# Optimization experiments

Hardware: AMD Instinct MI355X
Metric: run time of the kernel (lower is better)

The kernel has to match this reference:

```python
import jax, jax.numpy as jnp
import numpy as np
import math

B, T, C = 8, 1024, 1024
E, K = 8, 2
H = 4 * C


def new_gelu(x):
    # tanh-approx GELU, identical to the torch reference
    c = math.sqrt(2.0 / math.pi)
    return 0.5 * x * (1.0 + jnp.tanh(c * (x + 0.044715 * x ** 3)))


def setup_inputs() -> dict:
    key = jax.random.key(0)
    ks = jax.random.split(key, 4)
    x = jax.random.normal(ks[0], (B, T, C), dtype=jnp.float32)
    # router: nn.Linear(C, E, bias=False), weight [E, C], init std=0.02
    router_w = 0.02 * jax.random.normal(ks[1], (E, C), dtype=jnp.float32)
    # stacked expert MLP weights (bias=False): c_fc [E, C, H], c_proj [E, H, C]
    w_fc = 0.02 * jax.random.normal(ks[2], (E, C, H), dtype=jnp.float32)
    w_proj = 0.02 * jax.random.normal(ks[3], (E, H, C), dtype=jnp.float32)
    return {"x": x, "router_w": router_w, "w_fc": w_fc, "w_proj": w_proj}


def reference(x, router_w, w_fc, w_proj):
    n_expert = w_fc.shape[0]
    seq_rep = x.mean(axis=1)                                  # [B, C]
    router_logits = seq_rep @ router_w.T                      # [B, E]
    probs_full = jax.nn.softmax(router_logits.astype(jnp.float32), axis=-1)
    probs = probs_full.astype(x.dtype)
    weights, sel = jax.lax.top_k(probs, K)                    # [B, K]
    weights = weights / weights.sum(axis=-1, keepdims=True)

    # gather selected expert weights and run grouped dense MLPs
    w1 = w_fc[sel]                                            # [B, K, C, H]
    w2 = w_proj[sel]                                          # [B, K, H, C]
    h = new_gelu(jnp.einsum('btc,bkch->bkth', x, w1))         # [B, K, T, H]
    out_k = jnp.einsum('bkth,bkhc->bktc', h, w2)              # [B, K, T, C]
    final_output = jnp.einsum('bk,bktc->btc', weights, out_k)

    # load balancing loss
    Bf = jnp.asarray(x.shape[0], jnp.float32)
    expert_importance = probs_full.sum(axis=0) / Bf           # [E]
    is_assigned = jnp.zeros_like(probs_full).at[jnp.arange(x.shape[0])[:, None], sel].set(1.0)
    expert_load = is_assigned.sum(axis=0) / Bf                # [E]
    load_balancing_loss = n_expert * jnp.sum(expert_importance * expert_load)
    return final_output, load_balancing_loss
```

## Files before the change

kernel.cpp:

```cpp
#include <hip/hip_runtime.h>

#define B_ 8
#define T_ 1024
#define C_ 1024
#define E_ 8
#define H_ 4096

typedef float v4f __attribute__((ext_vector_type(4)));
typedef short v8s __attribute__((ext_vector_type(8)));

__device__ __forceinline__ unsigned short f2bf(float f) {
  union { float f; unsigned int u; } x; x.f = f;
  unsigned int r = x.u + 0x7fffu + ((x.u >> 16) & 1u);
  return (unsigned short)(r >> 16);
}

__device__ __forceinline__ void async_load16(const unsigned short* g, unsigned short* l) {
  __builtin_amdgcn_global_load_lds(
      (const __attribute__((address_space(1))) void*)g,
      (__attribute__((address_space(3))) void*)l, 16, 0, 0);
}


__global__ void k_meanpart(const float* __restrict__ x, float* __restrict__ part,
                           unsigned short* __restrict__ xb) {
  int b = blockIdx.x >> 5, tc = blockIdx.x & 31;
  int c4 = threadIdx.x * 4;
  const size_t base = (size_t)b * T_ * C_ + (size_t)tc * 32 * C_ + c4;
  const float* xp = x + base;
  v4f s = {0.f, 0.f, 0.f, 0.f};
  for (int t = 0; t < 32; ++t) {
    v4f v = *(const v4f*)(xp + (size_t)t * C_);
    s += v;
    ushort4 o;
    o.x = f2bf(v.x); o.y = f2bf(v.y); o.z = f2bf(v.z); o.w = f2bf(v.w);
    *(ushort4*)(xb + base + (size_t)t * C_) = o;
  }
  *(v4f*)(part + (size_t)(tc * B_ + b) * C_ + c4) = s;
}

__global__ void k_router(const float* __restrict__ part, const float* __restrict__ rw,
                         int* __restrict__ sel, float* __restrict__ wv,
                         float* __restrict__ loss_out) {
  __shared__ float seq[B_ * C_];
  __shared__ float red[B_ * E_][4];
  __shared__ float pr[B_][E_];
  __shared__ int ss[B_][2];
  const int tid = threadIdx.x;
  for (int idx = tid; idx < B_ * C_; idx += 256) {
    float s = 0.f;
#pragma unroll
    for (int tc = 0; tc < 32; ++tc) s += part[(size_t)tc * B_ * C_ + idx];
    seq[idx] = s * (1.0f / T_);
  }
  __syncthreads();
  {
    int pair = tid >> 2, sub = tid & 3;
    int b = pair >> 3, e = pair & 7;
    float acc = 0.f;
    const float* sp = seq + b * C_ + sub * 256;
    const float* wp = rw + e * C_ + sub * 256;
    for (int c = 0; c < 256; ++c) acc += sp[c] * wp[c];
    red[pair][sub] = acc;
  }
  __syncthreads();
  if (tid < B_ * E_)
    pr[tid >> 3][tid & 7] = red[tid][0] + red[tid][1] + red[tid][2] + red[tid][3];
  __syncthreads();
  if (tid < B_) {
    int b = tid;
    float mx = pr[b][0];
#pragma unroll
    for (int e = 1; e < E_; ++e) mx = fmaxf(mx, pr[b][e]);
    float p[E_]; float sum = 0.f;
#pragma unroll
    for (int e = 0; e < E_; ++e) { p[e] = __expf(pr[b][e] - mx); sum += p[e]; }
    float inv = 1.0f / sum;
#pragma unroll
    for (int e = 0; e < E_; ++e) { p[e] *= inv; pr[b][e] = p[e]; }
    int i0 = 0;
#pragma unroll
    for (int e = 1; e < E_; ++e) if (p[e] > p[i0]) i0 = e;
    int i1 = (i0 == 0) ? 1 : 0;
#pragma unroll
    for (int e = 0; e < E_; ++e) if (e != i0 && p[e] > p[i1]) i1 = e;
    float s2 = p[i0] + p[i1];
    sel[b * 2 + 0] = i0; sel[b * 2 + 1] = i1;
    wv[b * 2 + 0] = p[i0] / s2; wv[b * 2 + 1] = p[i1] / s2;
    ss[b][0] = i0; ss[b][1] = i1;
  }
  __syncthreads();
  if (tid == 0) {
    float loss = 0.f;
    for (int e = 0; e < E_; ++e) {
      float imp = 0.f, ld = 0.f;
      for (int b = 0; b < B_; ++b) {
        imp += pr[b][e];
        ld += ((ss[b][0] == e) || (ss[b][1] == e)) ? 1.f : 0.f;
      }
      loss += (imp / (float)B_) * (ld / (float)B_);
    }
    loss_out[0] = loss * (float)E_;
  }
}

__global__ void k_transpose(const float* __restrict__ src, unsigned short* __restrict__ dst,
                            int R, int Cc) {
  __shared__ float tile[64][65];
  const size_t sl = (size_t)blockIdx.z * R * Cc;
  int c0 = blockIdx.x * 64, r0 = blockIdx.y * 64;
  int tx = threadIdx.x & 15, ty = threadIdx.x >> 4;
#pragma unroll
  for (int p = 0; p < 4; ++p) {
    int r = p * 16 + ty;
    v4f v = *(const v4f*)(src + sl + (size_t)(r0 + r) * Cc + c0 + tx * 4);
    tile[r][tx * 4 + 0] = v.x; tile[r][tx * 4 + 1] = v.y;
    tile[r][tx * 4 + 2] = v.z; tile[r][tx * 4 + 3] = v.w;
  }
  __syncthreads();
#pragma unroll
  for (int p = 0; p < 4; ++p) {
    int c = p * 16 + ty;
    int rr = tx * 4;
    ushort4 o;
    o.x = f2bf(tile[rr + 0][c]); o.y = f2bf(tile[rr + 1][c]);
    o.z = f2bf(tile[rr + 2][c]); o.w = f2bf(tile[rr + 3][c]);
    *(ushort4*)(dst + sl + (size_t)(c0 + c) * R + r0 + rr) = o;
  }
}


__device__ __forceinline__ void gemm_seg(const unsigned short* A, int lda,
                                         const unsigned short* Bt, int ldb,
                                         int Kd, int row0, int col0,
                                         unsigned short* As, unsigned short* Bs,
                                         v4f (&acc)[4][4]) {
  const int tid = threadIdx.x;
  const int lane = tid & 63;
  const int wave = __builtin_amdgcn_readfirstlane(tid >> 6);
  const int r = lane & 15, q = lane >> 4;
  const int wm = wave & 1, wn = wave >> 1;
  const int qs = q ^ ((r >> 1) & 3);
  const int lrow = lane >> 2;
  const int lch = (lane & 3) ^ ((lane >> 3) & 3);
  const bool doA = (wave < 2);
  const int jb = (wave & 1) * 4;
  const int gld = doA ? lda : ldb;
  const unsigned short* gbase =
      (doA ? (A + (size_t)row0 * lda) : (Bt + (size_t)col0 * ldb)) +
      (size_t)(jb * 16 + lrow) * gld + lch * 8;
  unsigned short* lbase = (doA ? As : Bs) + jb * 512;

  for (int kc = 0; kc < Kd; kc += 32) {
    const unsigned short* g = gbase + kc;
    async_load16(g + 0 * 16 * (size_t)gld, lbase + 0 * 512);
    async_load16(g + 1 * 16 * (size_t)gld, lbase + 1 * 512);
    async_load16(g + 2 * 16 * (size_t)gld, lbase + 2 * 512);
    async_load16(g + 3 * 16 * (size_t)gld, lbase + 3 * 512);
    __syncthreads();
    v8s af[4], bf[4];
#pragma unroll
    for (int i = 0; i < 4; ++i)
      af[i] = *(const v8s*)&As[((wm * 64 + i * 16 + r) * 4 + qs) * 8];
#pragma unroll
    for (int j = 0; j < 4; ++j)
      bf[j] = *(const v8s*)&Bs[((wn * 64 + j * 16 + r) * 4 + qs) * 8];
#pragma unroll
    for (int i = 0; i < 4; ++i)
#pragma unroll
      for (int j = 0; j < 4; ++j)
        acc[i][j] = __builtin_amdgcn_mfma_f32_16x16x32_bf16(af[i], bf[j], acc[i][j], 0, 0, 0);
    __syncthreads();
  }
}

__global__ __launch_bounds__(256, 4) void k_gemm1(
    const unsigned short* __restrict__ Xb, const unsigned short* __restrict__ Wfct,
    const int* __restrict__ sel, const float* __restrict__ wv,
    unsigned short* __restrict__ Hout) {
  __shared__ unsigned short SH[128 * 64];
  unsigned short* As = SH;
  unsigned short* Bs = SH + 128 * 32;
  const int bk = blockIdx.z;
  const int e = sel[bk];
  const float wgt = wv[bk];
  const int row0 = blockIdx.y * 128, col0 = blockIdx.x * 128;
  v4f acc[4][4];
#pragma unroll
  for (int i = 0; i < 4; ++i)
#pragma unroll
    for (int j = 0; j < 4; ++j) acc[i][j] = (v4f){0.f, 0.f, 0.f, 0.f};

  gemm_seg(Xb + (size_t)(bk >> 1) * T_ * C_, C_, Wfct + (size_t)e * H_ * C_, C_,
           C_, row0, col0, As, Bs, acc);

  const int tid = threadIdx.x;
  const int lane = tid & 63;
  const int wave = tid >> 6;
  const int r = lane & 15, q = lane >> 4;
  const int wm = wave & 1, wn = wave >> 1;
  unsigned short* Co = Hout + (size_t)bk * T_ * H_;
#pragma unroll
  for (int hh = 0; hh < 2; ++hh) {
    if (wm == hh) {
#pragma unroll
      for (int i = 0; i < 4; ++i)
#pragma unroll
        for (int j = 0; j < 4; ++j)
#pragma unroll
          for (int p = 0; p < 4; ++p) {
            int lr = i * 16 + q * 4 + p;
            int lc = wn * 64 + j * 16 + r;
            float u = acc[i][j][p];
            float y = 0.7978845608028654f * (u + 0.044715f * u * u * u);
            float t = 1.0f - 2.0f / (__expf(2.0f * y) + 1.0f);
            SH[lr * 128 + lc] = f2bf(0.5f * u * (1.0f + t) * wgt);
          }
    }
    __syncthreads();
#pragma unroll
    for (int it = 0; it < 4; ++it) {
      int idx = it * 256 + tid;
      int row = idx >> 4, ch = idx & 15;
      *(v8s*)&Co[(size_t)(row0 + hh * 64 + row) * H_ + col0 + ch * 8] =
          *(const v8s*)&SH[row * 128 + ch * 8];
    }
    __syncthreads();
  }
}

__global__ __launch_bounds__(256, 4) void k_gemm2(
    const unsigned short* __restrict__ Hin, const unsigned short* __restrict__ Wpt,
    const int* __restrict__ sel, float* __restrict__ P0, float* __restrict__ P1) {
  __shared__ unsigned short SH[128 * 64];
  unsigned short* As = SH;
  unsigned short* Bs = SH + 128 * 32;
  const int bk = blockIdx.z;
  const int b = bk >> 1, k = bk & 1;
  const int e = sel[bk];
  const int row0 = blockIdx.y * 128, col0 = blockIdx.x * 128;
  v4f acc[4][4];
#pragma unroll
  for (int i = 0; i < 4; ++i)
#pragma unroll
    for (int j = 0; j < 4; ++j) acc[i][j] = (v4f){0.f, 0.f, 0.f, 0.f};

  gemm_seg(Hin + (size_t)bk * T_ * H_, H_, Wpt + (size_t)e * C_ * H_, H_,
           H_, row0, col0, As, Bs, acc);

  const int lane = threadIdx.x & 63;
  const int wave = threadIdx.x >> 6;
  const int r = lane & 15, q = lane >> 4;
  const int wm = wave & 1, wn = wave >> 1;
  float* Co = (k == 0 ? P0 : P1) + (size_t)b * T_ * C_;
#pragma unroll
  for (int i = 0; i < 4; ++i) {
    int gr = row0 + wm * 64 + i * 16 + q * 4;
#pragma unroll
    for (int j = 0; j < 4; ++j) {
      int gc = col0 + wn * 64 + j * 16 + r;
#pragma unroll
      for (int p = 0; p < 4; ++p)
        Co[(size_t)(gr + p) * C_ + gc] = acc[i][j][p];
    }
  }
}

__global__ void k_add(float* __restrict__ out, const float* __restrict__ p1) {
  size_t i = ((size_t)blockIdx.x * 256 + threadIdx.x) * 4;
  v4f a = *(const v4f*)(out + i);
  v4f b = *(const v4f*)(p1 + i);
  a += b;
  *(v4f*)(out + i) = a;
}


extern "C" void kernel_launch(void* const* d_in, const int* in_sizes, int n_in,
                              void* d_out, int out_size, void* d_ws, size_t ws_size,
                              hipStream_t stream) {
  const float* x   = (const float*)d_in[0];
  const float* rw  = (const float*)d_in[1];
  const float* wfc = (const float*)d_in[2];
  const float* wpj = (const float*)d_in[3];
  float* out = (float*)d_out;
  char* ws = (char*)d_ws;

  float*          part = (float*)(ws + 0);
  int*            sel  = (int*)(ws + 1048576);
  float*          wv   = (float*)(ws + 1048576 + 64);
  unsigned short* xb   = (unsigned short*)(ws + 2097152);
  unsigned short* wfct = (unsigned short*)(ws + 2097152 + 16777216);
  unsigned short* wpjt = (unsigned short*)(ws + 2097152 + 16777216 + 67108864);
  unsigned short* h    = (unsigned short*)(ws + 2097152 + 16777216 + 2*67108864ll);
  float*          p1   = (float*)(ws + 2097152);

  k_meanpart<<<dim3(B_ * 32), dim3(256), 0, stream>>>(x, part, xb);
  k_router<<<dim3(1), dim3(256), 0, stream>>>(part, rw, sel, wv,
                                              out + (size_t)B_ * T_ * C_);
  k_transpose<<<dim3(H_ / 64, C_ / 64, E_), dim3(256), 0, stream>>>(wfc, wfct, C_, H_);
  k_transpose<<<dim3(C_ / 64, H_ / 64, E_), dim3(256), 0, stream>>>(wpj, wpjt, H_, C_);

  k_gemm1<<<dim3(H_ / 128, T_ / 128, B_ * 2), dim3(256), 0, stream>>>(xb, wfct, sel, wv, h);
  k_gemm2<<<dim3(C_ / 128, T_ / 128, B_ * 2), dim3(256), 0, stream>>>(h, wpjt, sel, out, p1);
  k_add<<<dim3(B_ * T_ * C_ / 4 / 256), dim3(256), 0, stream>>>(out, p1);
}
```

Measured before the change: 757.9 us.

## Replace 128x128 GEMM tiles with double-buffered 256x256 tiles and block swizzle

Both expert GEMMs move from 128x128 tiles (256 threads, single-buffered K=32 steps) to 256x256 tiles with 512 threads, K=128 chunks and a double-buffered 128KB LDS ring. Global-to-LDS async loads for the next chunk are interleaved with MFMA quadrants using explicit vmcnt and lgkmcnt waits, barriers and setprio, so memory latency overlaps compute. Block indices are XCD-swizzled to improve L2 reuse of expert weights. The larger tiles cut redundant global traffic per FLOP, at the cost of fewer blocks (occupancy) and more fragile hand scheduling.

Measured after the change: 653.4 us. 13.8% less time.

```diff
diff --git a/kernel.cpp b/kernel.cpp
--- a/kernel.cpp
+++ b/kernel.cpp
@@ -130,135 +130,191 @@
 }
 
 
-__device__ __forceinline__ void gemm_seg(const unsigned short* A, int lda,
-                                         const unsigned short* Bt, int ldb,
-                                         int Kd, int row0, int col0,
-                                         unsigned short* As, unsigned short* Bs,
-                                         v4f (&acc)[4][4]) {
+#define BARv() __builtin_amdgcn_s_barrier()
+#define LGK0() asm volatile("s_waitcnt lgkmcnt(0)" ::: "memory")
+#define VMC4() asm volatile("s_waitcnt vmcnt(4)" ::: "memory")
+#define VMC0() asm volatile("s_waitcnt vmcnt(0)" ::: "memory")
+
+__device__ __forceinline__ void gemm256(const unsigned short* __restrict__ Ag,
+                                        const unsigned short* __restrict__ Bg,
+                                        int lda, int ldb, int Kd,
+                                        unsigned short* LDS, v4f (&acc)[8][4]) {
   const int tid = threadIdx.x;
   const int lane = tid & 63;
-  const int wave = __builtin_amdgcn_readfirstlane(tid >> 6);
-  const int r = lane & 15, q = lane >> 4;
-  const int wm = wave & 1, wn = wave >> 1;
-  const int qs = q ^ ((r >> 1) & 3);
-  const int lrow = lane >> 2;
-  const int lch = (lane & 3) ^ ((lane >> 3) & 3);
-  const bool doA = (wave < 2);
-  const int jb = (wave & 1) * 4;
-  const int gld = doA ? lda : ldb;
-  const unsigned short* gbase =
-      (doA ? (A + (size_t)row0 * lda) : (Bt + (size_t)col0 * ldb)) +
-      (size_t)(jb * 16 + lrow) * gld + lch * 8;
-  unsigned short* lbase = (doA ? As : Bs) + jb * 512;
-
-  for (int kc = 0; kc < Kd; kc += 32) {
-    const unsigned short* g = gbase + kc;
-    async_load16(g + 0 * 16 * (size_t)gld, lbase + 0 * 512);
-    async_load16(g + 1 * 16 * (size_t)gld, lbase + 1 * 512);
-    async_load16(g + 2 * 16 * (size_t)gld, lbase + 2 * 512);
-    async_load16(g + 3 * 16 * (size_t)gld, lbase + 3 * 512);
-    __syncthreads();
-    v8s af[4], bf[4];
-#pragma unroll
-    for (int i = 0; i < 4; ++i)
-      af[i] = *(const v8s*)&As[((wm * 64 + i * 16 + r) * 4 + qs) * 8];
-#pragma unroll
-    for (int j = 0; j < 4; ++j)
-      bf[j] = *(const v8s*)&Bs[((wn * 64 + j * 16 + r) * 4 + qs) * 8];
-#pragma unroll
-    for (int i = 0; i < 4; ++i)
-#pragma unroll
-      for (int j = 0; j < 4; ++j)
-        acc[i][j] = __builtin_amdgcn_mfma_f32_16x16x32_bf16(af[i], bf[j], acc[i][j], 0, 0, 0);
-    __syncthreads();
-  }
-}
-
-__global__ __launch_bounds__(256, 4) void k_gemm1(
+  const int w = __builtin_amdgcn_readfirstlane(tid >> 6);
+  const int wm = w >> 2, wn = w & 3;
+  const int rr = lane & 15, q = lane >> 4, s7 = rr & 7;
+  const int ck0 = (q ^ s7) * 8;
+  const int ck1 = ((4 | q) ^ s7) * 8;
+  const int aoff = wm * 8192 + rr * 64;
+  const int boff = 16384 + (wn >> 1) * 8192 + (wn & 1) * 4096 + rr * 64;
+  const int w8 = w * 8;
+  const int l3 = lane >> 3;
+  const int srow = w8 + l3;
+  const int sel8 = ((lane & 7) ^ l3) * 8;
+  v8s af[4][2], bfr[4][2];
+
+#define STG(gb, ld, reg) do { \
+    const unsigned short* _g = (gb) + (size_t)srow * (ld) + sel8; \
+    async_load16(_g, LDS + (reg) + w8 * 64); \
+    async_load16(_g + (size_t)64 * (ld), LDS + (reg) + 4096 + w8 * 64); \
+  } while (0)
+
+#define RDA(i2, qi, bs) do { \
+    af[i2][0] = *(const v8s*)&LDS[(bs) + aoff + ((qi)*4+(i2))*1024 + ck0]; \
+    af[i2][1] = *(const v8s*)&LDS[(bs) + aoff + ((qi)*4+(i2))*1024 + ck1]; \
+  } while (0)
+
+#define RDB(j, bs) do { \
+    bfr[j][0] = *(const v8s*)&LDS[(bs) + boff + (j)*1024 + ck0]; \
+    bfr[j][1] = *(const v8s*)&LDS[(bs) + boff + (j)*1024 + ck1]; \
+  } while (0)
+
+#define QUAD(qi, qj) do { \
+    __builtin_amdgcn_s_setprio(1); \
+    _Pragma("unroll") for (int _i = 0; _i < 4; ++_i) \
+    _Pragma("unroll") for (int _j = 0; _j < 2; ++_j) { \
+      acc[(qi)*4+_i][(qj)*2+_j] = __builtin_amdgcn_mfma_f32_16x16x32_bf16( \
+          af[_i][0], bfr[(qj)*2+_j][0], acc[(qi)*4+_i][(qj)*2+_j], 0, 0, 0); \
+      acc[(qi)*4+_i][(qj)*2+_j] = __builtin_amdgcn_mfma_f32_16x16x32_bf16( \
+          af[_i][1], bfr[(qj)*2+_j][1], acc[(qi)*4+_i][(qj)*2+_j], 0, 0, 0); \
+    } \
+    __builtin_amdgcn_s_setprio(0); \
+  } while (0)
+
+  STG(Ag, lda, 0);
+  STG(Ag + (size_t)128 * lda, lda, 8192);
+  STG(Bg, ldb, 16384);
+  STG(Bg + (size_t)128 * ldb, ldb, 24576);
+  STG(Bg + 64, ldb, 32768 + 16384);
+  STG(Bg + (size_t)128 * ldb + 64, ldb, 32768 + 24576);
+  VMC4();
+  BARv();
+
+  const int NI = Kd >> 7;
+  for (int I = 0; I < NI; ++I) {
+    const int k0 = I << 7;
+    const bool last = (I == NI - 1);
+    RDA(0,0,0); RDA(1,0,0); RDA(2,0,0); RDA(3,0,0); RDB(0,0); RDB(1,0);
+    STG(Ag + k0 + 64, lda, 32768 + 0);
+    BARv(); LGK0(); QUAD(0,0); BARv();
+    RDB(2,0); RDB(3,0);
+    STG(Ag + (size_t)128 * lda + k0 + 64, lda, 32768 + 8192);
+    BARv(); LGK0(); QUAD(0,1); BARv();
+    RDA(0,1,0); RDA(1,1,0); RDA(2,1,0); RDA(3,1,0);
+    if (!last) STG(Bg + k0 + 128, ldb, 16384);
+    BARv(); LGK0(); QUAD(1,0); BARv();
+    if (!last) STG(Bg + (size_t)128 * ldb + k0 + 128, ldb, 24576);
+    BARv(); LGK0(); QUAD(1,1);
+    if (last) { VMC0(); } else { VMC4(); }
+    BARv();
+    RDA(0,0,32768); RDA(1,0,32768); RDA(2,0,32768); RDA(3,0,32768);
+    RDB(0,32768); RDB(1,32768);
+    if (!last) STG(Ag + k0 + 128, lda, 0);
+    BARv(); LGK0(); QUAD(0,0); BARv();
+    RDB(2,32768); RDB(3,32768);
+    if (!last) STG(Ag + (size_t)128 * lda + k0 + 128, lda, 8192);
+    BARv(); LGK0(); QUAD(0,1); BARv();
+    RDA(0,1,32768); RDA(1,1,32768); RDA(2,1,32768); RDA(3,1,32768);
+    if (!last) STG(Bg + k0 + 192, ldb, 32768 + 16384);
+    BARv(); LGK0(); QUAD(1,0); BARv();
+    if (!last) STG(Bg + (size_t)128 * ldb + k0 + 192, ldb, 32768 + 24576);
+    BARv(); LGK0(); QUAD(1,1);
+    if (!last) VMC4();
+    BARv();
+  }
+#undef STG
+#undef RDA
+#undef RDB
+#undef QUAD
+}
+
+__global__ __launch_bounds__(512, 2) void k_gemm1(
     const unsigned short* __restrict__ Xb, const unsigned short* __restrict__ Wfct,
     const int* __restrict__ sel, const float* __restrict__ wv,
     unsigned short* __restrict__ Hout) {
-  __shared__ unsigned short SH[128 * 64];
-  unsigned short* As = SH;
-  unsigned short* Bs = SH + 128 * 32;
-  const int bk = blockIdx.z;
+  __shared__ unsigned short LDS[65536];
+  int flat = blockIdx.x + 16 * (blockIdx.y + 4 * blockIdx.z);
+  int swz = (flat & 7) * 128 + (flat >> 3);
+  const int bx = swz & 15, by = (swz >> 4) & 3, bk = swz >> 6;
   const int e = sel[bk];
   const float wgt = wv[bk];
-  const int row0 = blockIdx.y * 128, col0 = blockIdx.x * 128;
-  v4f acc[4][4];
-#pragma unroll
-  for (int i = 0; i < 4; ++i)
+  const int row0 = by * 256, col0 = bx * 256;
+  v4f acc[8][4];
+#pragma unroll
+  for (int i = 0; i < 8; ++i)
 #pragma unroll
     for (int j = 0; j < 4; ++j) acc[i][j] = (v4f){0.f, 0.f, 0.f, 0.f};
 
-  gemm_seg(Xb + (size_t)(bk >> 1) * T_ * C_, C_, Wfct + (size_t)e * H_ * C_, C_,
-           C_, row0, col0, As, Bs, acc);
+  gemm256(Xb + (size_t)(bk >> 1) * T_ * C_ + (size_t)row0 * C_,
+          Wfct + (size_t)e * H_ * C_ + (size_t)col0 * C_,
+          C_, C_, C_, LDS, acc);
 
   const int tid = threadIdx.x;
   const int lane = tid & 63;
-  const int wave = tid >> 6;
-  const int r = lane & 15, q = lane >> 4;
-  const int wm = wave & 1, wn = wave >> 1;
+  const int w = tid >> 6, wm = w >> 2, wn = w & 3;
+  const int rr = lane & 15, q = lane >> 4;
   unsigned short* Co = Hout + (size_t)bk * T_ * H_;
 #pragma unroll
-  for (int hh = 0; hh < 2; ++hh) {
-    if (wm == hh) {
-#pragma unroll
-      for (int i = 0; i < 4; ++i)
+  for (int h = 0; h < 2; ++h) {
+    if (wm == h) {
+#pragma unroll
+      for (int i = 0; i < 8; ++i)
 #pragma unroll
         for (int j = 0; j < 4; ++j)
 #pragma unroll
           for (int p = 0; p < 4; ++p) {
             int lr = i * 16 + q * 4 + p;
-            int lc = wn * 64 + j * 16 + r;
+            int lc = wn * 64 + j * 16 + rr;
             float u = acc[i][j][p];
             float y = 0.7978845608028654f * (u + 0.044715f * u * u * u);
             float t = 1.0f - 2.0f / (__expf(2.0f * y) + 1.0f);
-            SH[lr * 128 + lc] = f2bf(0.5f * u * (1.0f + t) * wgt);
+            LDS[lr * 272 + lc] = f2bf(0.5f * u * (1.0f + t) * wgt);
           }
     }
     __syncthreads();
 #pragma unroll
-    for (int it = 0; it < 4; ++it) {
-      int idx = it * 256 + tid;
-      int row = idx >> 4, ch = idx & 15;
-      *(v8s*)&Co[(size_t)(row0 + hh * 64 + row) * H_ + col0 + ch * 8] =
-          *(const v8s*)&SH[row * 128 + ch * 8];
+    for (int m = 0; m < 8; ++m) {
+      int idx = m * 512 + tid;
+      int row = idx >> 5, cc = idx & 31;
+      *(v8s*)&Co[(size_t)(row0 + h * 128 + row) * H_ + col0 + cc * 8] =
+          *(const v8s*)&LDS[row * 272 + cc * 8];
     }
     __syncthreads();
   }
 }
 
-__global__ __launch_bounds__(256, 4) void k_gemm2(
+__global__ __launch_bounds__(512, 2) void k_gemm2(
     const unsigned short* __restrict__ Hin, const unsigned short* __restrict__ Wpt,
     const int* __restrict__ sel, float* __restrict__ P0, float* __restrict__ P1) {
-  __shared__ unsigned short SH[128 * 64];
-  unsigned short* As = SH;
-  unsigned short* Bs = SH + 128 * 32;
-  const int bk = blockIdx.z;
+  __shared__ unsigned short LDS[65536];
+  int flat = blockIdx.x + 4 * (blockIdx.y + 4 * blockIdx.z);
+  int swz = (flat & 7) * 32 + (flat >> 3);
+  const int bx = swz & 3, by = (swz >> 2) & 3, bk = swz >> 4;
   const int b = bk >> 1, k = bk & 1;
   const int e = sel[bk];
-  const int row0 = blockIdx.y * 128, col0 = blockIdx.x * 128;
-  v4f acc[4][4];
-#pragma unroll
-  for (int i = 0; i < 4; ++i)
+  const int row0 = by * 256, col0 = bx * 256;
+  v4f acc[8][4];
+#pragma unroll
+  for (int i = 0; i < 8; ++i)
 #pragma unroll
     for (int j = 0; j < 4; ++j) acc[i][j] = (v4f){0.f, 0.f, 0.f, 0.f};
 
-  gemm_seg(Hin + (size_t)bk * T_ * H_, H_, Wpt + (size_t)e * C_ * H_, H_,
-           H_, row0, col0, As, Bs, acc);
-
-  const int lane = threadIdx.x & 63;
-  const int wave = threadIdx.x >> 6;
-  const int r = lane & 15, q = lane >> 4;
-  const int wm = wave & 1, wn = wave >> 1;
+  gemm256(Hin + (size_t)bk * T_ * H_ + (size_t)row0 * H_,
+          Wpt + (size_t)e * C_ * H_ + (size_t)col0 * H_,
+          H_, H_, H_, LDS, acc);
+
+  const int tid = threadIdx.x;
+  const int lane = tid & 63;
+  const int w = tid >> 6, wm = w >> 2, wn = w & 3;
+  const int rr = lane & 15, q = lane >> 4;
   float* Co = (k == 0 ? P0 : P1) + (size_t)b * T_ * C_;
 #pragma unroll
-  for (int i = 0; i < 4; ++i) {
-    int gr = row0 + wm * 64 + i * 16 + q * 4;
+  for (int i = 0; i < 8; ++i) {
+    int gr = row0 + wm * 128 + i * 16 + q * 4;
 #pragma unroll
     for (int j = 0; j < 4; ++j) {
-      int gc = col0 + wn * 64 + j * 16 + r;
+      int gc = col0 + wn * 64 + j * 16 + rr;
 #pragma unroll
       for (int p = 0; p < 4; ++p)
         Co[(size_t)(gr + p) * C_ + gc] = acc[i][j][p];
@@ -300,7 +356,7 @@
   k_transpose<<<dim3(H_ / 64, C_ / 64, E_), dim3(256), 0, stream>>>(wfc, wfct, C_, H_);
   k_transpose<<<dim3(C_ / 64, H_ / 64, E_), dim3(256), 0, stream>>>(wpj, wpjt, H_, C_);
 
-  k_gemm1<<<dim3(H_ / 128, T_ / 128, B_ * 2), dim3(256), 0, stream>>>(xb, wfct, sel, wv, h);
-  k_gemm2<<<dim3(C_ / 128, T_ / 128, B_ * 2), dim3(256), 0, stream>>>(h, wpjt, sel, out, p1);
+  k_gemm1<<<dim3(H_ / 256, T_ / 256, B_ * 2), dim3(512), 0, stream>>>(xb, wfct, sel, wv, h);
+  k_gemm2<<<dim3(C_ / 256, T_ / 256, B_ * 2), dim3(512), 0, stream>>>(h, wpjt, sel, out, p1);
   k_add<<<dim3(B_ * T_ * C_ / 4 / 256), dim3(256), 0, stream>>>(out, p1);
 }
```

## Rewrite expert GEMMs with triple-buffered 128x256 tiles and fused expert-sum

Applied to the files above, without the earlier changes.

The GEMM core moves to a 512-thread, 128x256-tile kernel with K-step 64. It triple-buffers LDS with async global-to-LDS loads, explicit vmcnt waits and sched barriers, double-buffers fragments, and raises MFMA priority. Block indices are swizzled for L2 locality. gemm2 now accumulates both selected experts into one accumulator in a single block, which removes the partial buffer and the separate add kernel. The cost is a large LDS footprint (144KB) that limits occupancy, and each gemm2 block does twice the K work.

Result: faster. 716.7 us (-5.4%).

```diff
diff --git a/kernel.cpp b/kernel.cpp
--- a/kernel.cpp
+++ b/kernel.cpp
@@ -130,148 +130,171 @@
 }
 
 
-__device__ __forceinline__ void gemm_seg(const unsigned short* A, int lda,
-                                         const unsigned short* Bt, int ldb,
-                                         int Kd, int row0, int col0,
-                                         unsigned short* As, unsigned short* Bs,
-                                         v4f (&acc)[4][4]) {
+#define BAR()  __builtin_amdgcn_s_barrier()
+#define SCH0() __builtin_amdgcn_sched_barrier(0)
+
+__device__ __forceinline__ void gemm_core(const unsigned short* __restrict__ Ag,
+                                          const unsigned short* __restrict__ Bg,
+                                          int lda, int ldb, int Kd,
+                                          unsigned short* LDS, v4f (&acc)[4][4]) {
   const int tid = threadIdx.x;
   const int lane = tid & 63;
-  const int wave = __builtin_amdgcn_readfirstlane(tid >> 6);
-  const int r = lane & 15, q = lane >> 4;
-  const int wm = wave & 1, wn = wave >> 1;
-  const int qs = q ^ ((r >> 1) & 3);
-  const int lrow = lane >> 2;
-  const int lch = (lane & 3) ^ ((lane >> 3) & 3);
-  const bool doA = (wave < 2);
-  const int jb = (wave & 1) * 4;
-  const int gld = doA ? lda : ldb;
-  const unsigned short* gbase =
-      (doA ? (A + (size_t)row0 * lda) : (Bt + (size_t)col0 * ldb)) +
-      (size_t)(jb * 16 + lrow) * gld + lch * 8;
-  unsigned short* lbase = (doA ? As : Bs) + jb * 512;
-
-  for (int kc = 0; kc < Kd; kc += 32) {
-    const unsigned short* g = gbase + kc;
-    async_load16(g + 0 * 16 * (size_t)gld, lbase + 0 * 512);
-    async_load16(g + 1 * 16 * (size_t)gld, lbase + 1 * 512);
-    async_load16(g + 2 * 16 * (size_t)gld, lbase + 2 * 512);
-    async_load16(g + 3 * 16 * (size_t)gld, lbase + 3 * 512);
-    __syncthreads();
-    v8s af[4], bf[4];
-#pragma unroll
-    for (int i = 0; i < 4; ++i)
-      af[i] = *(const v8s*)&As[((wm * 64 + i * 16 + r) * 4 + qs) * 8];
-#pragma unroll
-    for (int j = 0; j < 4; ++j)
-      bf[j] = *(const v8s*)&Bs[((wn * 64 + j * 16 + r) * 4 + qs) * 8];
-#pragma unroll
-    for (int i = 0; i < 4; ++i)
-#pragma unroll
-      for (int j = 0; j < 4; ++j)
-        acc[i][j] = __builtin_amdgcn_mfma_f32_16x16x32_bf16(af[i], bf[j], acc[i][j], 0, 0, 0);
-    __syncthreads();
-  }
-}
-
-__global__ __launch_bounds__(256, 4) void k_gemm1(
+  const int w = __builtin_amdgcn_readfirstlane(tid >> 6);
+  const int wm = w >> 2, wn = w & 3;
+  const int rr = lane & 15, q = lane >> 4, s7 = rr & 7;
+  const int ck0 = (q ^ s7) * 8, ck1 = ((4 | q) ^ s7) * 8;
+  const int aof0 = wm * 4096 + rr * 64;
+  const int aof1 = aof0 + 1024, aof2 = aof0 + 2048, aof3 = aof0 + 3072;
+  const int bof0 = 8192 + wn * 4096 + rr * 64;
+  const int bof1 = bof0 + 1024, bof2 = bof0 + 2048, bof3 = bof0 + 3072;
+  const int srow = tid >> 3;
+  const int sc8 = ((tid & 7) ^ (srow & 7)) * 8;
+  const int ldst = tid * 8;
+  v8s a0[4], b0[4], a1[4], b1[4];
+
+#define STG1(goff, ld, loff) async_load16((goff) + (size_t)srow * (ld) + sc8, LDS + (loff) + ldst)
+#define STG6(kof, bb) do { \
+    STG1(Ag + (kof), lda, (bb)); \
+    STG1(Ag + (size_t)64 * lda + (kof), lda, (bb) + 4096); \
+    STG1(Bg + (kof), ldb, (bb) + 8192); \
+    STG1(Bg + (size_t)64 * ldb + (kof), ldb, (bb) + 12288); \
+    STG1(Bg + (size_t)128 * ldb + (kof), ldb, (bb) + 16384); \
+    STG1(Bg + (size_t)192 * ldb + (kof), ldb, (bb) + 20480); \
+  } while (0)
+#define RD8(A_, B_, bb, CK) do { \
+    A_[0] = *(const v8s*)&LDS[(bb) + aof0 + (CK)]; \
+    A_[1] = *(const v8s*)&LDS[(bb) + aof1 + (CK)]; \
+    A_[2] = *(const v8s*)&LDS[(bb) + aof2 + (CK)]; \
+    A_[3] = *(const v8s*)&LDS[(bb) + aof3 + (CK)]; \
+    B_[0] = *(const v8s*)&LDS[(bb) + bof0 + (CK)]; \
+    B_[1] = *(const v8s*)&LDS[(bb) + bof1 + (CK)]; \
+    B_[2] = *(const v8s*)&LDS[(bb) + bof2 + (CK)]; \
+    B_[3] = *(const v8s*)&LDS[(bb) + bof3 + (CK)]; \
+  } while (0)
+#define MM16(A_, B_) do { __builtin_amdgcn_s_setprio(1); \
+    _Pragma("unroll") for (int i_ = 0; i_ < 4; ++i_) \
+    _Pragma("unroll") for (int j_ = 0; j_ < 4; ++j_) \
+      acc[i_][j_] = __builtin_amdgcn_mfma_f32_16x16x32_bf16(A_[i_], B_[j_], acc[i_][j_], 0, 0, 0); \
+    __builtin_amdgcn_s_setprio(0); } while (0)
+
+  STG6(0, 0);
+  STG6(64, 24576);
+  asm volatile("s_waitcnt vmcnt(6)" ::: "memory");
+  BAR(); SCH0();
+  RD8(a0, b0, 0, ck0);
+
+  int bb0 = 0, bb1 = 24576, bb2 = 49152;
+  const int NT = Kd >> 6;
+#pragma unroll 1
+  for (int t = 0; t < NT; ++t) {
+    const bool n1 = (t + 1 < NT), s2 = (t + 2 < NT);
+    RD8(a1, b1, bb0, ck1);
+    SCH0();
+    if (n1) asm volatile("s_waitcnt vmcnt(0)" ::: "memory");
+    BAR(); SCH0();
+    if (s2) STG6((t + 2) * 64, bb2);
+    MM16(a0, b0);
+    SCH0();
+    if (n1) RD8(a0, b0, bb1, ck0);
+    SCH0();
+    MM16(a1, b1);
+    SCH0();
+    int tmp = bb0; bb0 = bb1; bb1 = bb2; bb2 = tmp;
+  }
+#undef STG1
+#undef STG6
+#undef RD8
+#undef MM16
+}
+
+__global__ __launch_bounds__(512, 2) void k_gemm1(
     const unsigned short* __restrict__ Xb, const unsigned short* __restrict__ Wfct,
     const int* __restrict__ sel, const float* __restrict__ wv,
     unsigned short* __restrict__ Hout) {
-  __shared__ unsigned short SH[128 * 64];
-  unsigned short* As = SH;
-  unsigned short* Bs = SH + 128 * 32;
-  const int bk = blockIdx.z;
+  __shared__ unsigned short LDS[73728];
+  int flat = blockIdx.x + 16 * (blockIdx.y + 8 * blockIdx.z);
+  int swz = (flat & 7) * 256 + (flat >> 3);
+  const int bx = swz & 15, by = (swz >> 4) & 7, bk = swz >> 7;
   const int e = sel[bk];
   const float wgt = wv[bk];
-  const int row0 = blockIdx.y * 128, col0 = blockIdx.x * 128;
+  const int row0 = by * 128, col0 = bx * 256;
   v4f acc[4][4];
 #pragma unroll
   for (int i = 0; i < 4; ++i)
 #pragma unroll
     for (int j = 0; j < 4; ++j) acc[i][j] = (v4f){0.f, 0.f, 0.f, 0.f};
 
-  gemm_seg(Xb + (size_t)(bk >> 1) * T_ * C_, C_, Wfct + (size_t)e * H_ * C_, C_,
-           C_, row0, col0, As, Bs, acc);
+  gemm_core(Xb + (size_t)(bk >> 1) * T_ * C_ + (size_t)row0 * C_,
+            Wfct + (size_t)e * H_ * C_ + (size_t)col0 * C_,
+            C_, C_, C_, LDS, acc);
 
   const int tid = threadIdx.x;
   const int lane = tid & 63;
-  const int wave = tid >> 6;
-  const int r = lane & 15, q = lane >> 4;
-  const int wm = wave & 1, wn = wave >> 1;
+  const int w = tid >> 6, wm = w >> 2, wn = w & 3;
+  const int rr = lane & 15, q = lane >> 4;
   unsigned short* Co = Hout + (size_t)bk * T_ * H_;
-#pragma unroll
-  for (int hh = 0; hh < 2; ++hh) {
-    if (wm == hh) {
-#pragma unroll
-      for (int i = 0; i < 4; ++i)
-#pragma unroll
-        for (int j = 0; j < 4; ++j)
-#pragma unroll
-          for (int p = 0; p < 4; ++p) {
-            int lr = i * 16 + q * 4 + p;
-            int lc = wn * 64 + j * 16 + r;
-            float u = acc[i][j][p];
-            float y = 0.7978845608028654f * (u + 0.044715f * u * u * u);
-            float t = 1.0f - 2.0f / (__expf(2.0f * y) + 1.0f);
-            SH[lr * 128 + lc] = f2bf(0.5f * u * (1.0f + t) * wgt);
-          }
-    }
-    __syncthreads();
-#pragma unroll
-    for (int it = 0; it < 4; ++it) {
-      int idx = it * 256 + tid;
-      int row = idx >> 4, ch = idx & 15;
-      *(v8s*)&Co[(size_t)(row0 + hh * 64 + row) * H_ + col0 + ch * 8] =
-          *(const v8s*)&SH[row * 128 + ch * 8];
-    }
-    __syncthreads();
-  }
-}
-
-__global__ __launch_bounds__(256, 4) void k_gemm2(
+  __syncthreads();
+#pragma unroll
+  for (int i = 0; i < 4; ++i)
+#pragma unroll
+    for (int j = 0; j < 4; ++j)
+#pragma unroll
+      for (int p = 0; p < 4; ++p) {
+        int lr = wm * 64 + i * 16 + q * 4 + p;
+        int lc = wn * 64 + j * 16 + rr;
+        float u = acc[i][j][p];
+        float y = 0.7978845608028654f * (u + 0.044715f * u * u * u);
+        float t = 1.0f - 2.0f / (__expf(2.0f * y) + 1.0f);
+        LDS[lr * 264 + lc] = f2bf(0.5f * u * (1.0f + t) * wgt);
+      }
+  __syncthreads();
+#pragma unroll
+  for (int m = 0; m < 8; ++m) {
+    int idx = m * 512 + tid;
+    int row = idx >> 5, ch = idx & 31;
+    *(v8s*)&Co[(size_t)(row0 + row) * H_ + col0 + ch * 8] =
+        *(const v8s*)&LDS[row * 264 + ch * 8];
+  }
+}
+
+__global__ __launch_bounds__(512, 2) void k_gemm2(
     const unsigned short* __restrict__ Hin, const unsigned short* __restrict__ Wpt,
-    const int* __restrict__ sel, float* __restrict__ P0, float* __restrict__ P1) {
-  __shared__ unsigned short SH[128 * 64];
-  unsigned short* As = SH;
-  unsigned short* Bs = SH + 128 * 32;
-  const int bk = blockIdx.z;
-  const int b = bk >> 1, k = bk & 1;
-  const int e = sel[bk];
-  const int row0 = blockIdx.y * 128, col0 = blockIdx.x * 128;
+    const int* __restrict__ sel, float* __restrict__ out) {
+  __shared__ unsigned short LDS[73728];
+  int flat = blockIdx.x + 4 * (blockIdx.y + 8 * blockIdx.z);
+  int swz = (flat & 7) * 32 + (flat >> 3);
+  const int bx = swz & 3, by = (swz >> 2) & 7, b = swz >> 5;
+  const int row0 = by * 128, col0 = bx * 256;
   v4f acc[4][4];
 #pragma unroll
   for (int i = 0; i < 4; ++i)
 #pragma unroll
     for (int j = 0; j < 4; ++j) acc[i][j] = (v4f){0.f, 0.f, 0.f, 0.f};
 
-  gemm_seg(Hin + (size_t)bk * T_ * H_, H_, Wpt + (size_t)e * C_ * H_, H_,
-           H_, row0, col0, As, Bs, acc);
-
-  const int lane = threadIdx.x & 63;
-  const int wave = threadIdx.x >> 6;
-  const int r = lane & 15, q = lane >> 4;
-  const int wm = wave & 1, wn = wave >> 1;
-  float* Co = (k == 0 ? P0 : P1) + (size_t)b * T_ * C_;
+  gemm_core(Hin + (size_t)(2 * b) * T_ * H_ + (size_t)row0 * H_,
+            Wpt + (size_t)sel[2 * b] * C_ * H_ + (size_t)col0 * H_,
+            H_, H_, H_, LDS, acc);
+  __syncthreads();
+  gemm_core(Hin + (size_t)(2 * b + 1) * T_ * H_ + (size_t)row0 * H_,
+            Wpt + (size_t)sel[2 * b + 1] * C_ * H_ + (size_t)col0 * H_,
+            H_, H_, H_, LDS, acc);
+
+  const int tid = threadIdx.x;
+  const int lane = tid & 63;
+  const int w = tid >> 6, wm = w >> 2, wn = w & 3;
+  const int rr = lane & 15, q = lane >> 4;
+  float* Co = out + (size_t)b * T_ * C_;
 #pragma unroll
   for (int i = 0; i < 4; ++i) {
     int gr = row0 + wm * 64 + i * 16 + q * 4;
 #pragma unroll
     for (int j = 0; j < 4; ++j) {
-      int gc = col0 + wn * 64 + j * 16 + r;
+      int gc = col0 + wn * 64 + j * 16 + rr;
 #pragma unroll
       for (int p = 0; p < 4; ++p)
         Co[(size_t)(gr + p) * C_ + gc] = acc[i][j][p];
     }
   }
-}
-
-__global__ void k_add(float* __restrict__ out, const float* __restrict__ p1) {
-  size_t i = ((size_t)blockIdx.x * 256 + threadIdx.x) * 4;
-  v4f a = *(const v4f*)(out + i);
-  v4f b = *(const v4f*)(p1 + i);
-  a += b;
-  *(v4f*)(out + i) = a;
 }
 
 
@@ -292,7 +315,6 @@
   unsigned short* wfct = (unsigned short*)(ws + 2097152 + 16777216);
   unsigned short* wpjt = (unsigned short*)(ws + 2097152 + 16777216 + 67108864);
   unsigned short* h    = (unsigned short*)(ws + 2097152 + 16777216 + 2*67108864ll);
-  float*          p1   = (float*)(ws + 2097152);
 
   k_meanpart<<<dim3(B_ * 32), dim3(256), 0, stream>>>(x, part, xb);
   k_router<<<dim3(1), dim3(256), 0, stream>>>(part, rw, sel, wv,
@@ -300,7 +322,6 @@
   k_transpose<<<dim3(H_ / 64, C_ / 64, E_), dim3(256), 0, stream>>>(wfc, wfct, C_, H_);
   k_transpose<<<dim3(C_ / 64, H_ / 64, E_), dim3(256), 0, stream>>>(wpj, wpjt, H_, C_);
 
-  k_gemm1<<<dim3(H_ / 128, T_ / 128, B_ * 2), dim3(256), 0, stream>>>(xb, wfct, sel, wv, h);
-  k_gemm2<<<dim3(C_ / 128, T_ / 128, B_ * 2), dim3(256), 0, stream>>>(h, wpjt, sel, out, p1);
-  k_add<<<dim3(B_ * T_ * C_ / 4 / 256), dim3(256), 0, stream>>>(out, p1);
-}
+  k_gemm1<<<dim3(H_ / 256, T_ / 128, B_ * 2), dim3(512), 0, stream>>>(xb, wfct, sel, wv, h);
+  k_gemm2<<<dim3(C_ / 256, T_ / 128, B_), dim3(512), 0, stream>>>(h, wpjt, sel, out);
+}
```
